# Performance work log

Hardware: AMD Instinct MI355X
Metric: run time of the kernel (lower is better)

The kernel has to match this reference:

```python
import jax, jax.numpy as jnp
import numpy as np


def _smoothness_1d(x, k):
    # windows i in [0, N-k-1): smoothness = sum_j |x[i+j] - mean_j(x[i+j])|
    N = x.shape[0]
    W = N - k - 1  # matches range(N - k - 1) in the original loop
    idx = jnp.arange(W)[:, None] + jnp.arange(k)[None, :]  # [W, k]
    win = x[idx]  # [W, k] strided windows
    m = jnp.mean(win, axis=1, keepdims=True)
    return jnp.sum(jnp.abs(win - m), axis=1)  # [W]


def setup_inputs() -> dict:
    key = jax.random.key(0)
    k1, k2 = jax.random.split(key)
    N = 1000000
    yHat = jax.random.normal(k1, (N,), dtype=jnp.float32)
    y = jax.random.normal(k2, (N,), dtype=jnp.float32)
    return {"yHat": yHat, "y": y, "k": 64}


def reference(yHat, y, k):
    yHatSmooth = _smoothness_1d(yHat, k)
    ySmooth = _smoothness_1d(y, k)
    diff = yHatSmooth - ySmooth
    return jnp.mean(diff * diff)  # MSELoss (mean reduction)
```

## Files before the change

kernel.cpp:

```cpp
#include <hip/hip_runtime.h>


#define K     64
#define C     4
#define BLK   256
#define WPB   (BLK * C)
#define TILE  (WPB + K)
#define TILE4 (TILE / 4)

__device__ __forceinline__ void windows_saod(const float* s ,
                                             int o, float outd[C]) {
    float e[K + C];
    const float4* p = (const float4*)(s + o);
    #pragma unroll
    for (int i = 0; i < (K + C) / 4; ++i) {
        float4 t = p[i];
        e[4 * i + 0] = t.x; e[4 * i + 1] = t.y;
        e[4 * i + 2] = t.z; e[4 * i + 3] = t.w;
    }
    float a0 = 0.f, a1 = 0.f, a2 = 0.f, a3 = 0.f;
    #pragma unroll
    for (int j = 0; j < K; j += 4) {
        a0 += e[j + 0]; a1 += e[j + 1]; a2 += e[j + 2]; a3 += e[j + 3];
    }
    float sums[C];
    sums[0] = (a0 + a1) + (a2 + a3);
    #pragma unroll
    for (int c = 1; c < C; ++c)
        sums[c] = sums[c - 1] + (e[K + c - 1] - e[c - 1]);

    #pragma unroll
    for (int c = 0; c < C; ++c) {
        const float m = sums[c] * (1.0f / K);
        float d0 = 0.f, d1 = 0.f, d2 = 0.f, d3 = 0.f;
        #pragma unroll
        for (int j = 0; j < K; j += 4) {
            d0 += fabsf(e[c + j + 0] - m);
            d1 += fabsf(e[c + j + 1] - m);
            d2 += fabsf(e[c + j + 2] - m);
            d3 += fabsf(e[c + j + 3] - m);
        }
        outd[c] = (d0 + d1) + (d2 + d3);
    }
}

__global__ __launch_bounds__(BLK) void smoothness_loss_kernel(
    const float* __restrict__ yHat, const float* __restrict__ y,
    float* __restrict__ out, int N, int W, float invW)
{
    __shared__ __align__(16) float sA[TILE];
    __shared__ __align__(16) float sB[TILE];
    __shared__ float wave_sums[BLK / 64];

    const int base = blockIdx.x * WPB;
    const int tid  = threadIdx.x;

    const float4* gA = (const float4*)(yHat + base);
    const float4* gB = (const float4*)(y + base);
    const int g4max = (N - base) / 4;
    #pragma unroll
    for (int r = 0; r < 2; ++r) {
        const int i4 = tid + r * BLK;
        if (i4 < TILE4) {
            float4 a = make_float4(0.f, 0.f, 0.f, 0.f), b = a;
            if (i4 < g4max) { a = gA[i4]; b = gB[i4]; }
            ((float4*)sA)[i4] = a;
            ((float4*)sB)[i4] = b;
        }
    }
    __syncthreads();

    const int o  = tid * C;
    const int w0 = base + o;

    float dA[C], dB[C];
    windows_saod(sA, o, dA);
    windows_saod(sB, o, dB);

    float part = 0.f;
    #pragma unroll
    for (int c = 0; c < C; ++c) {
        if (w0 + c < W) {
            const float diff = dA[c] - dB[c];
            part += diff * diff;
        }
    }

    #pragma unroll
    for (int off = 32; off > 0; off >>= 1)
        part += __shfl_down(part, off, 64);

    const int lane = tid & 63;
    const int wv   = tid >> 6;
    if (lane == 0) wave_sums[wv] = part;
    __syncthreads();

    if (tid == 0) {
        float s = 0.f;
        #pragma unroll
        for (int i = 0; i < BLK / 64; ++i) s += wave_sums[i];
        atomicAdd(out, s * invW);
    }
}

extern "C" void kernel_launch(void* const* d_in, const int* in_sizes, int n_in,
                              void* d_out, int out_size, void* d_ws, size_t ws_size,
                              hipStream_t stream) {
    const float* yHat = (const float*)d_in[0];
    const float* y    = (const float*)d_in[1];
    float* out        = (float*)d_out;

    const int N = in_sizes[0];
    const int W = N - K - 1;
    const float invW = 1.0f / (float)W;

    hipMemsetAsync(out, 0, sizeof(float), stream);

    const int grid = (W + WPB - 1) / WPB;
    smoothness_loss_kernel<<<grid, BLK, 0, stream>>>(yHat, y, out, N, W, invW);
}
```

Baseline: 76.40 us.

## Split yHat and y window work across block halves with shared exchange

```diff
diff --git a/kernel.cpp b/kernel.cpp
--- a/kernel.cpp
+++ b/kernel.cpp
@@ -3,13 +3,13 @@
 
 #define K     64
 #define C     4
-#define BLK   256
-#define WPB   (BLK * C)
+#define HALF  128
+#define BLK   (2 * HALF)
+#define WPB   (HALF * C)
 #define TILE  (WPB + K)
 #define TILE4 (TILE / 4)
 
-__device__ __forceinline__ void windows_saod(const float* s ,
-                                             int o, float outd[C]) {
+__device__ __forceinline__ void windows_saod(const float* s, int o, float outd[C]) {
     float e[K + C];
     const float4* p = (const float4*)(s + o);
     #pragma unroll
@@ -44,12 +44,13 @@
     }
 }
 
-__global__ __launch_bounds__(BLK) void smoothness_loss_kernel(
+__global__ __launch_bounds__(BLK, 4) void smoothness_loss_kernel(
     const float* __restrict__ yHat, const float* __restrict__ y,
     float* __restrict__ out, int N, int W, float invW)
 {
     __shared__ __align__(16) float sA[TILE];
     __shared__ __align__(16) float sB[TILE];
+    __shared__ __align__(16) float4 xch[HALF];
     __shared__ float wave_sums[BLK / 64];
 
     const int base = blockIdx.x * WPB;
@@ -60,29 +61,41 @@
     const int g4max = (N - base) / 4;
     #pragma unroll
     for (int r = 0; r < 2; ++r) {
-        const int i4 = tid + r * BLK;
-        if (i4 < TILE4) {
-            float4 a = make_float4(0.f, 0.f, 0.f, 0.f), b = a;
-            if (i4 < g4max) { a = gA[i4]; b = gB[i4]; }
-            ((float4*)sA)[i4] = a;
-            ((float4*)sB)[i4] = b;
+        const int idx = tid + r * BLK;
+        if (idx < 2 * TILE4) {
+            const bool isB = (idx >= TILE4);
+            const int pos  = isB ? (idx - TILE4) : idx;
+            float4 v = make_float4(0.f, 0.f, 0.f, 0.f);
+            if (pos < g4max) v = isB ? gB[pos] : gA[pos];
+            float4* dst = isB ? (float4*)sB : (float4*)sA;
+            dst[pos] = v;
         }
     }
     __syncthreads();
 
-    const int o  = tid * C;
-    const int w0 = base + o;
+    const int half = tid >> 7;
+    const int lt   = tid & (HALF - 1);
+    const int o    = lt * C;
+    const float* s = half ? sB : sA;
 
-    float dA[C], dB[C];
-    windows_saod(sA, o, dA);
-    windows_saod(sB, o, dB);
+    float d[C];
+    windows_saod(s, o, d);
 
     float part = 0.f;
-    #pragma unroll
-    for (int c = 0; c < C; ++c) {
-        if (w0 + c < W) {
-            const float diff = dA[c] - dB[c];
-            part += diff * diff;
+    if (half) {
+        xch[lt] = make_float4(d[0], d[1], d[2], d[3]);
+    }
+    __syncthreads();
+    if (!half) {
+        const float4 db = xch[lt];
+        const float dBv[C] = {db.x, db.y, db.z, db.w};
+        const int w0 = base + o;
+        #pragma unroll
+        for (int c = 0; c < C; ++c) {
+            if (w0 + c < W) {
+                const float diff = d[c] - dBv[c];
+                part += diff * diff;
+            }
         }
     }
 
@@ -96,10 +109,10 @@
     __syncthreads();
 
     if (tid == 0) {
-        float s = 0.f;
+        float ssum = 0.f;
         #pragma unroll
-        for (int i = 0; i < BLK / 64; ++i) s += wave_sums[i];
-        atomicAdd(out, s * invW);
+        for (int i = 0; i < BLK / 64; ++i) ssum += wave_sums[i];
+        atomicAdd(out, ssum * invW);
     }
 }
 
```

Result: slower. 90.22 us (+18.1%).
